# Performance work log

Measured on AMD Instinct MI355X. Metric: run time of the kernel, lower is better.

## Reference

```python
import jax, jax.numpy as jnp
import numpy as np

L, NFEAT, J, S = 100000, 256, 128, 8  # nodes, features, hidden, samples_per_k


def setup_inputs() -> dict:
    key = jax.random.key(0)
    ks = jax.random.split(key, 8)
    X = jax.random.normal(ks[0], (L, NFEAT), dtype=jnp.float32)
    # sampled 2-permutation neighbor indices (first and second element of each permutation)
    idx0 = jax.random.randint(ks[1], (S, L), 0, L)
    idx1 = jax.random.randint(ks[2], (S, L), 0, L)
    def lin(k, fan_in, fan_out):
        bound = 1.0 / np.sqrt(fan_in)
        kw, kb = jax.random.split(k)
        W = jax.random.uniform(kw, (fan_in, fan_out), jnp.float32, -bound, bound)
        b = jax.random.uniform(kb, (fan_out,), jnp.float32, -bound, bound)
        return W, b
    W_h1, b_h1 = lin(ks[3], NFEAT, J)      # h1: Linear(nfeat, J)
    W_g1, b_g1 = lin(ks[4], 2 * J, J)      # g1: Linear(2J, J)
    W_f, b_f = lin(ks[5], J, 2)            # final1: Linear(J, 2)
    return {"X": X, "W_h1": W_h1, "b_h1": b_h1, "W_g1": W_g1, "b_g1": b_g1,
            "W_f": W_f, "b_f": b_f, "idx0": idx0, "idx1": idx1}


def reference(X, W_h1, b_h1, W_g1, b_g1, W_f, b_f, idx0, idx1):
    # h(x) = relu(h1(x)); since h is only ever applied to rows of X, compute once and gather.
    H = jax.nn.relu(X @ W_h1 + b_h1)                     # (L, J)
    # fk(k=2): mean over samples of g(cat(h(X[perm0]), h(X[perm1])))
    pair = jnp.concatenate([H[idx0], H[idx1]], axis=-1)  # (S, L, 2J) irregular gather
    E = jnp.mean(jax.nn.relu(pair @ W_g1 + b_g1), axis=0)  # (L, J)
    E = jax.nn.relu(E)                                   # relu of mean of relus (faithful)
    # E = g(cat(h(X), E))
    E = jax.nn.relu(jnp.concatenate([H, E], axis=-1) @ W_g1 + b_g1)  # (L, J)
    # yhat = final1(E)
    return E @ W_f + b_f                                 # (L, 2)
```

## Files before the change

kernel.cpp:

```cpp
#include <hip/hip_runtime.h>

#define L_NODES 100000
#define NFEAT   256
#define JDIM    128

typedef __bf16 bf16x8 __attribute__((ext_vector_type(8)));
typedef __bf16 bf16x4 __attribute__((ext_vector_type(4)));
typedef float  floatx4 __attribute__((ext_vector_type(4)));

__global__ __launch_bounds__(256) void k_prep(
    const float* __restrict__ Wh, const float* __restrict__ Wg,
    __bf16* __restrict__ WtH, __bf16* __restrict__ WtG2)
{
    int i = blockIdx.x * 256 + threadIdx.x;
    int n = i >> 8, k = i & 255;
    WtH[i] = (__bf16)Wh[k * JDIM + n];
    int n2 = i >> 7, k2 = i & 127;
    WtG2[i] = (n2 < 128) ? (__bf16)Wg[k2 * JDIM + n2]
                         : (__bf16)Wg[(128 + k2) * JDIM + (n2 - 128)];
}

__global__ __launch_bounds__(256) void k_h1uv(
    const float* __restrict__ X, const __bf16* __restrict__ WtH,
    const __bf16* __restrict__ WtG2, const float* __restrict__ b,
    __bf16* __restrict__ U, __bf16* __restrict__ V)
{
    __shared__ __bf16 Sm[64 * 264];

    const int tid  = threadIdx.x;
    const int row0 = blockIdx.x * 64;
    const int wave = tid >> 6, lane = tid & 63;
    const int lm = lane & 15, lq = lane >> 4;

    bf16x8 b1[2][8];
    #pragma unroll
    for (int nt = 0; nt < 2; ++nt) {
        int ntg = wave * 2 + nt;
        #pragma unroll
        for (int ks = 0; ks < 8; ++ks)
            b1[nt][ks] = *(const bf16x8*)(WtH + (size_t)(ntg * 16 + lm) * 256 + ks * 32 + lq * 8);
    }

    #pragma unroll
    for (int it = 0; it < 16; ++it) {
        int f4  = it * 256 + tid;
        int row = f4 >> 6, c4 = f4 & 63;
        int grow = row0 + row; if (grow >= L_NODES) grow = L_NODES - 1;
        float4 v = *(const float4*)(X + (size_t)grow * NFEAT + c4 * 4);
        bf16x4 o; o[0]=(__bf16)v.x; o[1]=(__bf16)v.y; o[2]=(__bf16)v.z; o[3]=(__bf16)v.w;
        *(bf16x4*)&Sm[row * 264 + c4 * 4] = o;
    }
    __syncthreads();

    floatx4 acc1[4][2] = {};
    #pragma unroll
    for (int ks = 0; ks < 8; ++ks) {
        bf16x8 af[4];
        #pragma unroll
        for (int t = 0; t < 4; ++t)
            af[t] = *(const bf16x8*)&Sm[(t * 16 + lm) * 264 + ks * 32 + lq * 8];
        #pragma unroll
        for (int t = 0; t < 4; ++t)
            #pragma unroll
            for (int nt = 0; nt < 2; ++nt)
                acc1[t][nt] = __builtin_amdgcn_mfma_f32_16x16x32_bf16(
                    af[t], b1[nt][ks], acc1[t][nt], 0, 0, 0);
    }

    bf16x8 b2[4][4];
    #pragma unroll
    for (int nt = 0; nt < 4; ++nt) {
        int ntg = wave * 4 + nt;
        #pragma unroll
        for (int ks = 0; ks < 4; ++ks)
            b2[nt][ks] = *(const bf16x8*)(WtG2 + (size_t)(ntg * 16 + lm) * 128 + ks * 32 + lq * 8);
    }

    __syncthreads();

    #pragma unroll
    for (int nt = 0; nt < 2; ++nt) {
        int col = (wave * 2 + nt) * 16 + lm;
        float bias = b[col];
        #pragma unroll
        for (int t = 0; t < 4; ++t)
            #pragma unroll
            for (int p = 0; p < 4; ++p)
                Sm[(t * 16 + lq * 4 + p) * 136 + col] =
                    (__bf16)fmaxf(acc1[t][nt][p] + bias, 0.f);
    }
    __syncthreads();

    floatx4 acc2[4][4] = {};
    #pragma unroll
    for (int ks = 0; ks < 4; ++ks) {
        bf16x8 af[4];
        #pragma unroll
        for (int t = 0; t < 4; ++t)
            af[t] = *(const bf16x8*)&Sm[(t * 16 + lm) * 136 + ks * 32 + lq * 8];
        #pragma unroll
        for (int t = 0; t < 4; ++t)
            #pragma unroll
            for (int nt = 0; nt < 4; ++nt)
                acc2[t][nt] = __builtin_amdgcn_mfma_f32_16x16x32_bf16(
                    af[t], b2[nt][ks], acc2[t][nt], 0, 0, 0);
    }

    __syncthreads();

    #pragma unroll
    for (int nt = 0; nt < 4; ++nt) {
        int col = (wave * 4 + nt) * 16 + lm;
        #pragma unroll
        for (int t = 0; t < 4; ++t)
            #pragma unroll
            for (int p = 0; p < 4; ++p)
                Sm[(t * 16 + lq * 4 + p) * 264 + col] = (__bf16)acc2[t][nt][p];
    }
    __syncthreads();

    #pragma unroll
    for (int it = 0; it < 8; ++it) {
        int fid = it * 256 + tid;
        int row = fid >> 5, c8 = fid & 31;
        int grow = row0 + row;
        if (grow < L_NODES) {
            int col = c8 * 8;
            bf16x8 v = *(bf16x8*)&Sm[row * 264 + col];
            if (col < 128) *(bf16x8*)(U + (size_t)grow * JDIM + col) = v;
            else           *(bf16x8*)(V + (size_t)grow * JDIM + (col - 128)) = v;
        }
    }
}

__global__ __launch_bounds__(256) void k_gfinal(
    const __bf16* __restrict__ U, const __bf16* __restrict__ V,
    const __bf16* __restrict__ WtGv, const float* __restrict__ bg,
    const float* __restrict__ Wf, const float* __restrict__ bf,
    const int* __restrict__ idx0, const int* __restrict__ idx1,
    float* __restrict__ out)
{
    __shared__ int    sidx0[8][64], sidx1[8][64];
    __shared__ __bf16 E1s[64 * 136];
    __shared__ __bf16 Us [64 * 136];
    __shared__ float  part[4][64][2];

    const int tid  = threadIdx.x;
    const int row0 = blockIdx.x * 64;
    const int wave = tid >> 6, lane = tid & 63;
    const int lm = lane & 15, lq = lane >> 4;

    bf16x8 b3[2][4];
    #pragma unroll
    for (int nt = 0; nt < 2; ++nt) {
        int ntg = wave * 2 + nt;
        #pragma unroll
        for (int ks = 0; ks < 4; ++ks)
            b3[nt][ks] = *(const bf16x8*)(WtGv + (size_t)(ntg * 16 + lm) * 128 + ks * 32 + lq * 8);
    }

    #pragma unroll
    for (int it = 0; it < 4; ++it) {
        int fid = it * 256 + tid;
        int m = fid >> 9, rem = fid & 511;
        int s = rem >> 6, il = rem & 63;
        int gr = row0 + il; if (gr >= L_NODES) gr = L_NODES - 1;
        int val = (m ? idx1 : idx0)[(size_t)s * L_NODES + gr];
        if (m) sidx1[s][il] = val; else sidx0[s][il] = val;
    }
    #pragma unroll
    for (int it = 0; it < 4; ++it) {
        int fid = it * 256 + tid;
        int r = fid >> 4, c8 = fid & 15;
        int g = row0 + r; if (g >= L_NODES) g = L_NODES - 1;
        *(bf16x8*)&Us[r * 136 + c8 * 8] = *(const bf16x8*)(U + (size_t)g * JDIM + c8 * 8);
    }
    __syncthreads();

    {
        const int c0 = (tid & 15) * 8;
        const int rb = tid >> 4;
        float bias[8];
        *(float4*)&bias[0] = *(const float4*)(bg + c0);
        *(float4*)&bias[4] = *(const float4*)(bg + c0 + 4);

        float acc[4][8] = {};
        #pragma unroll
        for (int s = 0; s < 8; ++s) {
            #pragma unroll
            for (int rr = 0; rr < 4; ++rr) {
                int r = rb + rr * 16;
                int a0 = sidx0[s][r], a1 = sidx1[s][r];
                bf16x8 u = *(const bf16x8*)(U + (size_t)a0 * JDIM + c0);
                bf16x8 v = *(const bf16x8*)(V + (size_t)a1 * JDIM + c0);
                #pragma unroll
                for (int p = 0; p < 8; ++p)
                    acc[rr][p] += fmaxf((float)u[p] + (float)v[p] + bias[p], 0.f);
            }
        }
        #pragma unroll
        for (int rr = 0; rr < 4; ++rr) {
            int r = rb + rr * 16;
            bf16x8 o;
            #pragma unroll
            for (int p = 0; p < 8; ++p)
                o[p] = (__bf16)fmaxf(acc[rr][p] * 0.125f, 0.f);
            *(bf16x8*)&E1s[r * 136 + c0] = o;
        }
    }
    __syncthreads();

    floatx4 acc[4][2] = {};
    #pragma unroll
    for (int ks = 0; ks < 4; ++ks) {
        bf16x8 af[4];
        #pragma unroll
        for (int t = 0; t < 4; ++t)
            af[t] = *(const bf16x8*)&E1s[(t * 16 + lm) * 136 + ks * 32 + lq * 8];
        #pragma unroll
        for (int t = 0; t < 4; ++t)
            #pragma unroll
            for (int nt = 0; nt < 2; ++nt)
                acc[t][nt] = __builtin_amdgcn_mfma_f32_16x16x32_bf16(
                    af[t], b3[nt][ks], acc[t][nt], 0, 0, 0);
    }

    float bias[2], wf0[2], wf1[2];
    #pragma unroll
    for (int nt = 0; nt < 2; ++nt) {
        int col = (wave * 2 + nt) * 16 + lm;
        bias[nt] = bg[col];
        wf0[nt] = Wf[col * 2 + 0];
        wf1[nt] = Wf[col * 2 + 1];
    }
    #pragma unroll
    for (int t = 0; t < 4; ++t) {
        float p0[4], p1[4];
        #pragma unroll
        for (int p = 0; p < 4; ++p) {
            int r = t * 16 + lq * 4 + p;
            float a0 = 0.f, a1 = 0.f;
            #pragma unroll
            for (int nt = 0; nt < 2; ++nt) {
                int col = (wave * 2 + nt) * 16 + lm;
                float e2 = fmaxf((float)Us[r * 136 + col] + acc[t][nt][p] + bias[nt], 0.f);
                a0 = fmaf(e2, wf0[nt], a0);
                a1 = fmaf(e2, wf1[nt], a1);
            }
            p0[p] = a0; p1[p] = a1;
        }
        #pragma unroll
        for (int m = 1; m <= 8; m <<= 1)
            #pragma unroll
            for (int p = 0; p < 4; ++p) {
                p0[p] += __shfl_xor(p0[p], m, 16);
                p1[p] += __shfl_xor(p1[p], m, 16);
            }
        if (lm == 0)
            #pragma unroll
            for (int p = 0; p < 4; ++p) {
                part[wave][t * 16 + lq * 4 + p][0] = p0[p];
                part[wave][t * 16 + lq * 4 + p][1] = p1[p];
            }
    }
    __syncthreads();

    if (tid < 128) {
        int row = tid >> 1, o = tid & 1;
        int grow = row0 + row;
        if (grow < L_NODES)
            out[(size_t)grow * 2 + o] =
                part[0][row][o] + part[1][row][o] + part[2][row][o] + part[3][row][o] + bf[o];
    }
}

extern "C" void kernel_launch(void* const* d_in, const int* in_sizes, int n_in,
                              void* d_out, int out_size, void* d_ws, size_t ws_size,
                              hipStream_t stream) {
    const float* X    = (const float*)d_in[0];
    const float* W_h1 = (const float*)d_in[1];
    const float* b_h1 = (const float*)d_in[2];
    const float* W_g1 = (const float*)d_in[3];
    const float* b_g1 = (const float*)d_in[4];
    const float* W_f  = (const float*)d_in[5];
    const float* b_f  = (const float*)d_in[6];
    const int*   idx0 = (const int*)d_in[7];
    const int*   idx1 = (const int*)d_in[8];
    float* out = (float*)d_out;

    __bf16* U    = (__bf16*)d_ws;
    __bf16* V    = U   + (size_t)L_NODES * JDIM;
    __bf16* WtH  = V   + (size_t)L_NODES * JDIM;
    __bf16* WtG2 = WtH + 32768;
    __bf16* WtGv = WtG2 + 128 * 128;

    k_prep<<<128, 256, 0, stream>>>(W_h1, W_g1, WtH, WtG2);
    k_h1uv<<<(L_NODES + 63) / 64, 256, 0, stream>>>(X, WtH, WtG2, b_h1, U, V);
    k_gfinal<<<(L_NODES + 63) / 64, 256, 0, stream>>>(U, V, WtGv, b_g1, W_f, b_f,
                                                      idx0, idx1, out);
}
```

Baseline: 268.5 us.

## Double-buffer gather loads and cut register and LDS pressure in k_gfinal

```diff
diff --git a/kernel.cpp b/kernel.cpp
--- a/kernel.cpp
+++ b/kernel.cpp
@@ -133,31 +133,22 @@
     }
 }
 
-__global__ __launch_bounds__(256) void k_gfinal(
+__global__ __launch_bounds__(256, 4) void k_gfinal(
     const __bf16* __restrict__ U, const __bf16* __restrict__ V,
     const __bf16* __restrict__ WtGv, const float* __restrict__ bg,
     const float* __restrict__ Wf, const float* __restrict__ bf,
     const int* __restrict__ idx0, const int* __restrict__ idx1,
     float* __restrict__ out)
 {
-    __shared__ int    sidx0[8][64], sidx1[8][64];
+    __shared__ int    sidx[2][8][64];
     __shared__ __bf16 E1s[64 * 136];
     __shared__ __bf16 Us [64 * 136];
-    __shared__ float  part[4][64][2];
+    float (*part)[64][2] = (float (*)[64][2])&sidx[0][0][0];
 
     const int tid  = threadIdx.x;
     const int row0 = blockIdx.x * 64;
     const int wave = tid >> 6, lane = tid & 63;
     const int lm = lane & 15, lq = lane >> 4;
-
-    bf16x8 b3[2][4];
-    #pragma unroll
-    for (int nt = 0; nt < 2; ++nt) {
-        int ntg = wave * 2 + nt;
-        #pragma unroll
-        for (int ks = 0; ks < 4; ++ks)
-            b3[nt][ks] = *(const bf16x8*)(WtGv + (size_t)(ntg * 16 + lm) * 128 + ks * 32 + lq * 8);
-    }
 
     #pragma unroll
     for (int it = 0; it < 4; ++it) {
@@ -165,8 +156,7 @@
         int m = fid >> 9, rem = fid & 511;
         int s = rem >> 6, il = rem & 63;
         int gr = row0 + il; if (gr >= L_NODES) gr = L_NODES - 1;
-        int val = (m ? idx1 : idx0)[(size_t)s * L_NODES + gr];
-        if (m) sidx1[s][il] = val; else sidx0[s][il] = val;
+        sidx[m][s][il] = (m ? idx1 : idx0)[(size_t)s * L_NODES + gr];
     }
     #pragma unroll
     for (int it = 0; it < 4; ++it) {
@@ -185,19 +175,37 @@
         *(float4*)&bias[4] = *(const float4*)(bg + c0 + 4);
 
         float acc[4][8] = {};
-        #pragma unroll
-        for (int s = 0; s < 8; ++s) {
+        bf16x8 uA[4], vA[4], uB[4], vB[4];
+
+        auto LOADP = [&](int s, bf16x8 (&uu)[4], bf16x8 (&vv)[4]) {
             #pragma unroll
             for (int rr = 0; rr < 4; ++rr) {
                 int r = rb + rr * 16;
-                int a0 = sidx0[s][r], a1 = sidx1[s][r];
-                bf16x8 u = *(const bf16x8*)(U + (size_t)a0 * JDIM + c0);
-                bf16x8 v = *(const bf16x8*)(V + (size_t)a1 * JDIM + c0);
+                int a0 = sidx[0][s][r], a1 = sidx[1][s][r];
+                uu[rr] = *(const bf16x8*)(U + (size_t)a0 * JDIM + c0);
+                vv[rr] = *(const bf16x8*)(V + (size_t)a1 * JDIM + c0);
+            }
+        };
+        auto ACCUM = [&](bf16x8 (&uu)[4], bf16x8 (&vv)[4]) {
+            #pragma unroll
+            for (int rr = 0; rr < 4; ++rr)
                 #pragma unroll
                 for (int p = 0; p < 8; ++p)
-                    acc[rr][p] += fmaxf((float)u[p] + (float)v[p] + bias[p], 0.f);
+                    acc[rr][p] += fmaxf((float)uu[rr][p] + (float)vv[rr][p] + bias[p], 0.f);
+        };
+
+        LOADP(0, uA, vA);
+        #pragma unroll
+        for (int s = 0; s < 8; ++s) {
+            if ((s & 1) == 0) {
+                if (s < 7) LOADP(s + 1, uB, vB);
+                ACCUM(uA, vA);
+            } else {
+                if (s < 7) LOADP(s + 1, uA, vA);
+                ACCUM(uB, vB);
             }
         }
+
         #pragma unroll
         for (int rr = 0; rr < 4; ++rr) {
             int r = rb + rr * 16;
@@ -209,6 +217,15 @@
         }
     }
     __syncthreads();
+
+    bf16x8 b3[2][4];
+    #pragma unroll
+    for (int nt = 0; nt < 2; ++nt) {
+        int ntg = wave * 2 + nt;
+        #pragma unroll
+        for (int ks = 0; ks < 4; ++ks)
+            b3[nt][ks] = *(const bf16x8*)(WtGv + (size_t)(ntg * 16 + lm) * 128 + ks * 32 + lq * 8);
+    }
 
     floatx4 acc[4][2] = {};
     #pragma unroll
```

Result: no change. 266.3 us (-0.8%).
